# Kernel optimization log

Hardware: AMD Instinct MI355X
Metric: run time of the kernel (lower is better)

Reference implementation:

```python
import jax, jax.numpy as jnp
import numpy as np

DIM = 768
HEAD = 12


def setup_inputs() -> dict:
    key = jax.random.key(0)
    ks = jax.random.split(key, 7)
    B, N, C = 4, 2048, DIM
    s = 0.02
    return {
        "x": jax.random.normal(ks[0], (B, N, C), dtype=jnp.float32),
        "wq": jax.random.normal(ks[1], (C, C), dtype=jnp.float32) * s,
        "bq": jax.random.normal(ks[2], (C,), dtype=jnp.float32) * s,
        "wkv": jax.random.normal(ks[3], (C, 2 * C), dtype=jnp.float32) * s,
        "bkv": jax.random.normal(ks[4], (2 * C,), dtype=jnp.float32) * s,
        "wp": jax.random.normal(ks[5], (C, C), dtype=jnp.float32) * s,
        "bp": jax.random.normal(ks[6], (C,), dtype=jnp.float32) * s,
    }


def reference(x, wq, bq, wkv, bkv, wp, bp):
    B, N, C = x.shape
    H = HEAD
    D = C // H
    scale = D ** -0.5
    # projections
    q = (x @ wq + bq).reshape(B, N, H, D)          # [B,N,H,D]
    kv = (x @ wkv + bkv).reshape(B, N, 2, H, D)
    k = kv[:, :, 0]                                 # [B,N,H,D]
    v = kv[:, :, 1]
    # attention scores [B,H,N,N]
    attn = jnp.einsum('bnhd,bmhd->bhnm', q, k) * scale
    attn = jax.nn.softmax(attn, axis=-1)
    x_atten = jnp.einsum('bhnm,bmhd->bnhd', attn, v).reshape(B, N, C)
    return x_atten @ wp + bp
```

## Files before the change

### kernel.cpp

```cpp
#include <hip/hip_runtime.h>

typedef unsigned short u16;
typedef __attribute__((ext_vector_type(8))) short bf16x8;
typedef __attribute__((ext_vector_type(4))) float f32x4;

#define MFMA(a, b, c) __builtin_amdgcn_mfma_f32_16x16x32_bf16(a, b, c, 0, 0, 0)
#define LOG2E 1.44269504088896340736f

__device__ __forceinline__ u16 f2bf(float f) {
    union { float f; unsigned u; } v; v.f = f;
    unsigned r = v.u + 0x7fffu + ((v.u >> 16) & 1u);
    return (u16)(r >> 16);
}
__device__ __forceinline__ float bf2f(u16 h) {
    union { unsigned u; float f; } v; v.u = ((unsigned)h) << 16;
    return v.f;
}
__device__ __forceinline__ unsigned pkbf(float a, float b) {
#if __has_builtin(__builtin_amdgcn_cvt_pk_bf16_f32)
    typedef __attribute__((ext_vector_type(2))) __bf16 bf2_t;
    bf2_t v = __builtin_amdgcn_cvt_pk_bf16_f32(a, b);
    return __builtin_bit_cast(unsigned, v);
#else
    return (unsigned)f2bf(a) | ((unsigned)f2bf(b) << 16);
#endif
}
__device__ __forceinline__ float ex2(float x) {
#if __has_builtin(__builtin_amdgcn_exp2f)
    return __builtin_amdgcn_exp2f(x);
#else
    return exp2f(x);
#endif
}
__device__ __forceinline__ bf16x8 frag_from(unsigned a, unsigned b, unsigned c, unsigned d) {
    uint4 v; v.x = a; v.y = b; v.z = c; v.w = d;
    return __builtin_bit_cast(bf16x8, v);
}

__device__ __forceinline__ void g2l16(const void* g, void* lds_base) {
    __builtin_amdgcn_global_load_lds(
        (const __attribute__((address_space(1))) unsigned*)(unsigned long long)(uintptr_t)g,
        (__attribute__((address_space(3))) unsigned*)(unsigned)(uintptr_t)lds_base,
        16, 0, 0);
}

__global__ __launch_bounds__(256) void prep_kernel(
    const float* __restrict__ x, const float* __restrict__ wq,
    const float* __restrict__ wkv, const float* __restrict__ wp,
    u16* __restrict__ xb, u16* __restrict__ wtqkv, u16* __restrict__ wtp)
{
    int bz = blockIdx.x;
    int t = threadIdx.x;
    if (bz < 6144) {
        int i = (bz * 256 + t) * 4;
        float4 v = *(const float4*)&x[i];
        uint2 o;
        o.x = pkbf(v.x, v.y);
        o.y = pkbf(v.z, v.w);
        *(uint2*)&xb[i] = o;
        return;
    }
    __shared__ float tile[32][33];
    const float* W; u16* Wt; int cols; int r = bz - 6144;
    if (r < 576)       { W = wq;  Wt = wtqkv;             cols = 768;  }
    else if (r < 1728) { W = wkv; Wt = wtqkv + 768 * 768; cols = 1536; r -= 576; }
    else               { W = wp;  Wt = wtp;               cols = 768;  r -= 1728; }
    int nbx = cols / 32;
    int bx = (r % nbx) * 32, by = (r / nbx) * 32;
    int tx = t & 31, ty = t >> 5;
    for (int i = 0; i < 4; i++)
        tile[ty + 8 * i][tx] = W[(size_t)(by + ty + 8 * i) * cols + bx + tx];
    __syncthreads();
    for (int i = 0; i < 4; i++)
        Wt[(size_t)(bx + ty + 8 * i) * 768 + by + tx] = f2bf(tile[tx][ty + 8 * i]);
}

__global__ __launch_bounds__(256, 4) void gemm128(
    const u16* __restrict__ A, const u16* __restrict__ Bt,
    const float* __restrict__ bias0, const float* __restrict__ bias1, int bsplit,
    u16* __restrict__ outB, u16* __restrict__ vtg, int M, int N, int K)
{
    __shared__ __align__(16) u16 smem[17408];
    u16* As = smem;
    u16* Bs = smem + 8192;
    u16* Cs = smem;

    int gid = blockIdx.x;
    int bmi = ((gid & 7) << 3) | ((gid >> 3) & 7);
    int bni = gid >> 6;
    int bm = bmi * 128, bn = bni * 128;

    int t = threadIdx.x;
    int w = t >> 6, l = t & 63, q4 = l >> 4, lm = l & 15, lm7 = l & 7;
    int wm = (w >> 1) * 64, wn = (w & 1) * 64;

    f32x4 acc[4][4];
    for (int i = 0; i < 4; i++) for (int j = 0; j < 4; j++) acc[i][j] = (f32x4){0, 0, 0, 0};

    int srow = l >> 3;
    int schunk = (l & 7) ^ srow;

    for (int kt = 0; kt < K; kt += 64) {
        for (int p = 0; p < 4; p++) {
            int row = p * 32 + w * 8 + srow;
            g2l16(&A [(size_t)(bm + row) * K + kt + schunk * 8], &As[(p * 32 + w * 8) * 64]);
            g2l16(&Bt[(size_t)(bn + row) * K + kt + schunk * 8], &Bs[(p * 32 + w * 8) * 64]);
        }
        __syncthreads();
        for (int kc = 0; kc < 2; kc++) {
            bf16x8 a[4], b[4];
            for (int i = 0; i < 4; i++)
                a[i] = *(const bf16x8*)&As[(wm + 16 * i + lm) * 64 + ((4 * kc + q4) ^ lm7) * 8];
            for (int j = 0; j < 4; j++)
                b[j] = *(const bf16x8*)&Bs[(wn + 16 * j + lm) * 64 + ((4 * kc + q4) ^ lm7) * 8];
            for (int i = 0; i < 4; i++)
                for (int j = 0; j < 4; j++)
                    acc[i][j] = MFMA(a[i], b[j], acc[i][j]);
        }
        __syncthreads();
    }

    if (bn < 1536) {
        for (int i = 0; i < 4; i++)
            for (int j = 0; j < 4; j++) {
                int col = bn + wn + 16 * j + lm;
                float bv = (col < bsplit) ? bias0[col] : bias1[col - bsplit];
                for (int r = 0; r < 4; r++)
                    Cs[(wm + 16 * i + 4 * q4 + r) * 132 + wn + 16 * j + lm] =
                        f2bf(acc[i][j][r] + bv);
            }
        __syncthreads();
        int row = t >> 1, c0 = (t & 1) * 8;
        for (int s = 0; s < 8; s++)
            *(uint4*)&outB[(size_t)(bm + row) * N + bn + c0 + s * 16] =
                *(const uint4*)&Cs[row * 132 + c0 + s * 16];
    } else {
        for (int i = 0; i < 4; i++)
            for (int j = 0; j < 4; j++) {
                int cl = wn + 16 * j + lm;
                float bv = bias1[bn + cl - bsplit];
                uint2 pk;
                pk.x = pkbf(acc[i][j][0] + bv, acc[i][j][1] + bv);
                pk.y = pkbf(acc[i][j][2] + bv, acc[i][j][3] + bv);
                *(uint2*)&Cs[cl * 132 + wm + 16 * i + 4 * q4] = pk;
            }
        __syncthreads();
        int c = t >> 1, half = t & 1;
        int d = c & 63, hloc = c >> 6;
        int b = bm >> 11;
        int bh = b * 12 + ((bn - 1536) >> 6) + hloc;
        size_t rowoff = ((size_t)bh * 64 + d) * 2048 + (bm & 2047) + half * 64;
        const u16* base = &Cs[c * 132 + half * 64];
        for (int oct = 0; oct < 8; oct++) {
            int n0 = 32 * (oct >> 2) + 4 * (oct & 3);
            uint2 lo = *(const uint2*)&base[n0];
            uint2 hi = *(const uint2*)&base[n0 + 16];
            uint4 o; o.x = lo.x; o.y = lo.y; o.z = hi.x; o.w = hi.y;
            *(uint4*)&vtg[rowoff + oct * 8] = o;
        }
    }
}

__global__ __launch_bounds__(256, 4) void gemm_n64(
    const u16* __restrict__ A, const u16* __restrict__ Bt,
    const float* __restrict__ bias, float* __restrict__ outF, int M, int N, int K)
{
    __shared__ __align__(16) u16 smem[12288];
    u16* As = smem;
    u16* Bs = smem + 8192;
    float* Cf = (float*)smem;

    int gid = blockIdx.x;
    int bmi = ((gid & 7) << 3) | ((gid >> 3) & 7);
    int bni = gid >> 6;
    int bm = bmi * 128, bn = bni * 64;

    int t = threadIdx.x;
    int w = t >> 6, l = t & 63, q4 = l >> 4, lm = l & 15, lm7 = l & 7;
    int wm = (w >> 1) * 64, wn = (w & 1) * 32;

    f32x4 acc[4][2];
    for (int i = 0; i < 4; i++) for (int j = 0; j < 2; j++) acc[i][j] = (f32x4){0, 0, 0, 0};

    int srow = l >> 3;
    int schunk = (l & 7) ^ srow;

    for (int kt = 0; kt < K; kt += 64) {
        for (int p = 0; p < 4; p++) {
            int row = p * 32 + w * 8 + srow;
            g2l16(&A[(size_t)(bm + row) * K + kt + schunk * 8], &As[(p * 32 + w * 8) * 64]);
        }
        for (int p = 0; p < 2; p++) {
            int row = p * 32 + w * 8 + srow;
            g2l16(&Bt[(size_t)(bn + row) * K + kt + schunk * 8], &Bs[(p * 32 + w * 8) * 64]);
        }
        __syncthreads();
        for (int kc = 0; kc < 2; kc++) {
            bf16x8 a[4], b[2];
            for (int i = 0; i < 4; i++)
                a[i] = *(const bf16x8*)&As[(wm + 16 * i + lm) * 64 + ((4 * kc + q4) ^ lm7) * 8];
            for (int j = 0; j < 2; j++)
                b[j] = *(const bf16x8*)&Bs[(wn + 16 * j + lm) * 64 + ((4 * kc + q4) ^ lm7) * 8];
            for (int i = 0; i < 4; i++)
                for (int j = 0; j < 2; j++)
                    acc[i][j] = MFMA(a[i], b[j], acc[i][j]);
        }
        __syncthreads();
    }

    for (int round = 0; round < 2; round++) {
        if (round) __syncthreads();
        if ((w >> 1) == round) {
            for (int i = 0; i < 4; i++)
                for (int j = 0; j < 2; j++) {
                    int cl = wn + 16 * j + lm;
                    float bv = bias[bn + cl];
                    for (int r = 0; r < 4; r++)
                        Cf[(16 * i + 4 * q4 + r) * 68 + cl] = acc[i][j][r] + bv;
                }
        }
        __syncthreads();
        int row = t >> 4, c4 = (t & 15) * 4;
        for (int s = 0; s < 4; s++) {
            int rr = row + s * 16;
            *(float4*)&outF[(size_t)(bm + round * 64 + rr) * N + bn + c4] =
                *(const float4*)&Cf[rr * 68 + c4];
        }
    }
}

__global__ __launch_bounds__(256, 3) void attn_kernel(const u16* __restrict__ qkv,
                                                      const u16* __restrict__ vtg,
                                                      u16* __restrict__ xatt)
{
    __shared__ __align__(16) u16 smem[16384];

    int gid = blockIdx.x;
    int bh = gid % 48, qt = gid / 48;
    int b = bh / 12, h = bh % 12;

    int t = threadIdx.x;
    int w = t >> 6, l = t & 63, q4 = l >> 4, lm = l & 15, lm7 = l & 7;
    int qw = qt * 128 + w * 32;
    size_t rowbase = (size_t)b * 2048;

    int srow = l >> 3;
    int schunk = (l & 7) ^ srow;
    const u16* kp[2];
    const u16* vp[2];
    for (int p = 0; p < 2; p++) {
        int row = w * 16 + p * 8 + srow;
        kp[p] = &qkv[(rowbase + row) * 2304 + 768 + h * 64 + schunk * 8];
        vp[p] = &vtg[((size_t)bh * 64 + row) * 2048 + schunk * 8];
    }

    bf16x8 qf[2][2];
    for (int qi = 0; qi < 2; qi++) {
        size_t row = rowbase + qw + 16 * qi + lm;
        for (int kq = 0; kq < 2; kq++) {
            bf16x8 raw = *(const bf16x8*)&qkv[row * 2304 + h * 64 + kq * 32 + q4 * 8];
            bf16x8 sc;
            for (int j = 0; j < 8; j++) sc[j] = (short)f2bf(bf2f((u16)raw[j]) * (0.125f * LOG2E));
            qf[qi][kq] = sc;
        }
    }

    const bf16x8 ONES = frag_from(0x3F803F80u, 0x3F803F80u, 0x3F803F80u, 0x3F803F80u);

    int offA = lm * 64 + (q4 ^ lm7) * 8;
    int offB = lm * 64 + ((4 | q4) ^ lm7) * 8;

    f32x4 acc[2][4];
    f32x4 acc_l[2];
    for (int qi = 0; qi < 2; qi++) {
        for (int dt = 0; dt < 4; dt++) acc[qi][dt] = (f32x4){0, 0, 0, 0};
        acc_l[qi] = (f32x4){0, 0, 0, 0};
    }

    for (int p = 0; p < 2; p++) {
        g2l16(kp[p], smem + (w * 16 + p * 8) * 64);
        g2l16(vp[p], smem + 8192 + (w * 16 + p * 8) * 64);
    }

    const size_t KSTEP = (size_t)64 * 2304;
    for (int it = 0; it < 32; it++) {
        __syncthreads();
        int buf = it & 1;
        if (it + 1 < 32) {
            int nbuf = buf ^ 1;
            for (int p = 0; p < 2; p++) {
                kp[p] += KSTEP;
                vp[p] += 64;
                g2l16(kp[p], smem + nbuf * 4096 + (w * 16 + p * 8) * 64);
                g2l16(vp[p], smem + 8192 + nbuf * 4096 + (w * 16 + p * 8) * 64);
            }
        }
        const u16* Kb = smem + buf * 4096;
        const u16* Vb = smem + 8192 + buf * 4096;

        f32x4 s[2][4];
        for (int kt2 = 0; kt2 < 4; kt2++) {
            bf16x8 kf0 = *(const bf16x8*)&Kb[kt2 * 1024 + offA];
            bf16x8 kf1 = *(const bf16x8*)&Kb[kt2 * 1024 + offB];
            __builtin_amdgcn_s_setprio(1);
            for (int qi = 0; qi < 2; qi++) {
                f32x4 z = {0, 0, 0, 0};
                z = MFMA(kf0, qf[qi][0], z);
                z = MFMA(kf1, qf[qi][1], z);
                s[qi][kt2] = z;
            }
            __builtin_amdgcn_s_setprio(0);
        }

        bf16x8 vf0[4], vf1[4];
        for (int dt = 0; dt < 4; dt++) {
            vf0[dt] = *(const bf16x8*)&Vb[dt * 1024 + offA];
            vf1[dt] = *(const bf16x8*)&Vb[dt * 1024 + offB];
        }

        for (int qi = 0; qi < 2; qi++) {
            uint2 pk[4];
            for (int kt2 = 0; kt2 < 4; kt2++) {
                float p0 = ex2(s[qi][kt2][0]);
                float p1 = ex2(s[qi][kt2][1]);
                float p2 = ex2(s[qi][kt2][2]);
                float p3 = ex2(s[qi][kt2][3]);
                pk[kt2].x = pkbf(p0, p1);
                pk[kt2].y = pkbf(p2, p3);
            }

            bf16x8 af0 = frag_from(pk[0].x, pk[0].y, pk[1].x, pk[1].y);
            bf16x8 af1 = frag_from(pk[2].x, pk[2].y, pk[3].x, pk[3].y);
            __builtin_amdgcn_s_setprio(1);
            for (int dt = 0; dt < 4; dt++) {
                acc[qi][dt] = MFMA(af0, vf0[dt], acc[qi][dt]);
                acc[qi][dt] = MFMA(af1, vf1[dt], acc[qi][dt]);
            }
            acc_l[qi] = MFMA(af0, ONES, acc_l[qi]);
            acc_l[qi] = MFMA(af1, ONES, acc_l[qi]);
            __builtin_amdgcn_s_setprio(0);
        }
    }

    for (int qi = 0; qi < 2; qi++) {
        float ar[4];
        for (int r = 0; r < 4; r++) ar[r] = 1.0f / acc_l[qi][r];
        for (int dt = 0; dt < 4; dt++)
            for (int r = 0; r < 4; r++) {
                int row = qw + 16 * qi + 4 * q4 + r;
                xatt[(rowbase + row) * 768 + h * 64 + 16 * dt + lm] =
                    f2bf(acc[qi][dt][r] * ar[r]);
            }
    }
}

extern "C" void kernel_launch(void* const* d_in, const int* in_sizes, int n_in,
                              void* d_out, int out_size, void* d_ws, size_t ws_size,
                              hipStream_t stream)
{
    const float* x   = (const float*)d_in[0];
    const float* wq  = (const float*)d_in[1];
    const float* bq  = (const float*)d_in[2];
    const float* wkv = (const float*)d_in[3];
    const float* bkv = (const float*)d_in[4];
    const float* wp  = (const float*)d_in[5];
    const float* bp  = (const float*)d_in[6];
    float* out = (float*)d_out;

    char* ws = (char*)d_ws;
    u16* xb    = (u16*)(ws);
    u16* wtqkv = (u16*)(ws + 12582912);
    u16* wtp   = (u16*)(ws + 16121856);
    u16* qkvb  = (u16*)(ws + 17301504);
    u16* xatt  = (u16*)(ws + 55050240);
    u16* vtg   = (u16*)(ws + 67632128);

    prep_kernel<<<8448, 256, 0, stream>>>(x, wq, wkv, wp, xb, wtqkv, wtp);

    gemm128<<<1152, 256, 0, stream>>>(
        xb, wtqkv, bq, bkv, 768, qkvb, vtg, 8192, 2304, 768);

    attn_kernel<<<768, 256, 0, stream>>>(qkvb, vtg, xatt);

    gemm_n64<<<768, 256, 0, stream>>>(
        xatt, wtp, bp, out, 8192, 768, 768);
}
```

Before: 208.1 us.

## Load V fragments directly from global memory instead of staging through LDS

The attention kernel now reads each V tile straight from global memory into registers at the top of each iteration, removing the LDS double-buffer for V and halving shared memory to 8192 elements. The packed bf16 conversion is also forced to inline asm v_cvt_pk_bf16_f32. This cuts LDS traffic and LDS footprint, which may allow more resident blocks. The cost is that global load latency is exposed inside the loop with no prefetch, and each wave issues uncoalesced-ish per-lane global loads that other waves also repeat.

```diff
diff --git a/kernel.cpp b/kernel.cpp
--- a/kernel.cpp
+++ b/kernel.cpp
@@ -17,13 +17,9 @@
     return v.f;
 }
 __device__ __forceinline__ unsigned pkbf(float a, float b) {
-#if __has_builtin(__builtin_amdgcn_cvt_pk_bf16_f32)
-    typedef __attribute__((ext_vector_type(2))) __bf16 bf2_t;
-    bf2_t v = __builtin_amdgcn_cvt_pk_bf16_f32(a, b);
-    return __builtin_bit_cast(unsigned, v);
-#else
-    return (unsigned)f2bf(a) | ((unsigned)f2bf(b) << 16);
-#endif
+    unsigned r;
+    asm("v_cvt_pk_bf16_f32 %0, %1, %2" : "=v"(r) : "v"(a), "v"(b));
+    return r;
 }
 __device__ __forceinline__ float ex2(float x) {
 #if __has_builtin(__builtin_amdgcn_exp2f)
@@ -233,7 +229,7 @@
                                                       const u16* __restrict__ vtg,
                                                       u16* __restrict__ xatt)
 {
-    __shared__ __align__(16) u16 smem[16384];
+    __shared__ __align__(16) u16 smem[8192];
 
     int gid = blockIdx.x;
     int bh = gid % 48, qt = gid / 48;
@@ -247,12 +243,14 @@
     int srow = l >> 3;
     int schunk = (l & 7) ^ srow;
     const u16* kp[2];
-    const u16* vp[2];
     for (int p = 0; p < 2; p++) {
         int row = w * 16 + p * 8 + srow;
         kp[p] = &qkv[(rowbase + row) * 2304 + 768 + h * 64 + schunk * 8];
-        vp[p] = &vtg[((size_t)bh * 64 + row) * 2048 + schunk * 8];
-    }
+    }
+    const u16* vp0 = &vtg[((size_t)bh * 64 +  0 + lm) * 2048 + q4 * 8];
+    const u16* vp1 = &vtg[((size_t)bh * 64 + 16 + lm) * 2048 + q4 * 8];
+    const u16* vp2 = &vtg[((size_t)bh * 64 + 32 + lm) * 2048 + q4 * 8];
+    const u16* vp3 = &vtg[((size_t)bh * 64 + 48 + lm) * 2048 + q4 * 8];
 
     bf16x8 qf[2][2];
     for (int qi = 0; qi < 2; qi++) {
@@ -277,26 +275,29 @@
         acc_l[qi] = (f32x4){0, 0, 0, 0};
     }
 
-    for (int p = 0; p < 2; p++) {
+    for (int p = 0; p < 2; p++)
         g2l16(kp[p], smem + (w * 16 + p * 8) * 64);
-        g2l16(vp[p], smem + 8192 + (w * 16 + p * 8) * 64);
-    }
 
     const size_t KSTEP = (size_t)64 * 2304;
     for (int it = 0; it < 32; it++) {
         __syncthreads();
         int buf = it & 1;
+
+        bf16x8 vf0[4], vf1[4];
+        vf0[0] = *(const bf16x8*)(vp0);      vf1[0] = *(const bf16x8*)(vp0 + 32);
+        vf0[1] = *(const bf16x8*)(vp1);      vf1[1] = *(const bf16x8*)(vp1 + 32);
+        vf0[2] = *(const bf16x8*)(vp2);      vf1[2] = *(const bf16x8*)(vp2 + 32);
+        vf0[3] = *(const bf16x8*)(vp3);      vf1[3] = *(const bf16x8*)(vp3 + 32);
+        vp0 += 64; vp1 += 64; vp2 += 64; vp3 += 64;
+
         if (it + 1 < 32) {
             int nbuf = buf ^ 1;
             for (int p = 0; p < 2; p++) {
                 kp[p] += KSTEP;
-                vp[p] += 64;
                 g2l16(kp[p], smem + nbuf * 4096 + (w * 16 + p * 8) * 64);
-                g2l16(vp[p], smem + 8192 + nbuf * 4096 + (w * 16 + p * 8) * 64);
             }
         }
         const u16* Kb = smem + buf * 4096;
-        const u16* Vb = smem + 8192 + buf * 4096;
 
         f32x4 s[2][4];
         for (int kt2 = 0; kt2 < 4; kt2++) {
@@ -312,12 +313,6 @@
             __builtin_amdgcn_s_setprio(0);
         }
 
-        bf16x8 vf0[4], vf1[4];
-        for (int dt = 0; dt < 4; dt++) {
-            vf0[dt] = *(const bf16x8*)&Vb[dt * 1024 + offA];
-            vf1[dt] = *(const bf16x8*)&Vb[dt * 1024 + offB];
-        }
-
         for (int qi = 0; qi < 2; qi++) {
             uint2 pk[4];
             for (int kt2 = 0; kt2 < 4; kt2++) {
```

Measured after the change: 244.0 us. +17.2%, slower.
